# Kernel optimization log

Measured on AMD Instinct MI355X. Metric: run time of the kernel, lower is better.

The kernel has to match this reference:

```python
import jax, jax.numpy as jnp
import numpy as np

B, N, H, E, D = 8, 2048, 1024, 8, 2048


def setup_inputs() -> dict:
    key = jax.random.key(0)
    k = jax.random.split(key, 5)
    x = jax.random.normal(k[0], (B, N, H), dtype=jnp.float32)
    Wr = jax.random.normal(k[1], (H, E), dtype=jnp.float32) * 0.02
    br = jnp.zeros((E,), dtype=jnp.float32)
    W1 = jax.random.normal(k[2], (E, H, D), dtype=jnp.float32) * 0.02
    b1 = jnp.zeros((E, D), dtype=jnp.float32)
    W2 = jax.random.normal(k[3], (E, D, H), dtype=jnp.float32) * 0.02
    b2 = jnp.zeros((E, H), dtype=jnp.float32)
    return {"x": x, "Wr": Wr, "br": br, "W1": W1, "b1": b1, "W2": W2, "b2": b2}


def reference(x, Wr, br, W1, b1, W2, b2):
    # x: [B,N,H]; router v1, top-1, eval mode (no expert dropout)
    Bx, Nx, Hx = x.shape
    Ex = Wr.shape[1]
    x_flat = x.reshape(Bx * Nx, Hx)                      # [T,H]
    logits = x_flat @ Wr + br                            # [T,E]
    probs = jax.nn.softmax(logits, axis=-1)              # [T,E]
    expert_idx = jnp.argmax(probs, axis=-1)              # [T]

    out_flat = jnp.zeros_like(x_flat)
    for e in range(Ex):  # small fixed loop over experts
        h = jax.nn.gelu(x_flat @ W1[e] + b1[e], approximate=False)  # exact erf GELU (torch default)
        eout = h @ W2[e] + b2[e]                         # [T,H]
        out_flat = jnp.where((expert_idx == e)[:, None], eout, out_flat)

    out = x + out_flat.reshape(Bx, Nx, Hx)               # residual

    p_i = probs.mean(axis=0)                             # [E]
    balance_loss = Ex * jnp.sum(p_i ** 2)
    EPS = 1e-8
    entropy = -jnp.sum(probs * jnp.log(probs + EPS), axis=-1)
    entropy_loss = entropy.mean()
    tokens_per_expert = jnp.bincount(expert_idx, length=Ex)
    return out, balance_loss, entropy_loss, tokens_per_expert
```

## Files before the change

kernel.cpp:

```cpp
#include <hip/hip_runtime.h>
#include <math.h>

#define TT 16384
#define HH 1024
#define DD 2048
#define EE 8
#define MAXT 96

typedef float f32x4 __attribute__((ext_vector_type(4)));
typedef __bf16 bf16x8 __attribute__((ext_vector_type(8)));

__device__ __forceinline__ unsigned short f2bf(float f) {
  union { float f; unsigned u; } v; v.f = f;
  unsigned r = v.u + 0x7FFFu + ((v.u >> 16) & 1u);
  return (unsigned short)(r >> 16);
}

__device__ __forceinline__ void gl2lds16(const unsigned short* g, unsigned short* l) {
  __builtin_amdgcn_global_load_lds(
      (const __attribute__((address_space(1))) void*)g,
      (__attribute__((address_space(3))) void*)l, 16, 0, 0);
}

__global__ void k_init(int* counts, float* probs_sum, float* ent_sum) {
  int t = threadIdx.x;
  if (t < EE) { counts[t] = 0; probs_sum[t] = 0.f; }
  if (t == 0) *ent_sum = 0.f;
}

__global__ __launch_bounds__(256) void k_transpose(const float* __restrict__ src,
                                                   unsigned short* __restrict__ dst,
                                                   int R, int C) {
  __shared__ float tile[32][33];
  int tilesC = C / 32, tilesR = R / 32;
  int bid = blockIdx.x;
  int e = bid / (tilesR * tilesC);
  int rem = bid % (tilesR * tilesC);
  int tr = rem / tilesC, tc = rem % tilesC;
  const float* s = src + (size_t)e * R * C;
  unsigned short* d = dst + (size_t)e * R * C;
  int tx = threadIdx.x & 31, ty = threadIdx.x >> 5;
#pragma unroll
  for (int i = 0; i < 4; ++i)
    tile[ty + i * 8][tx] = s[(size_t)(tr * 32 + ty + i * 8) * C + tc * 32 + tx];
  __syncthreads();
#pragma unroll
  for (int i = 0; i < 4; ++i) {
    int rr = ty + i * 8;
    d[(size_t)(tc * 32 + rr) * R + tr * 32 + tx] = f2bf(tile[tx][rr]);
  }
}

__global__ __launch_bounds__(256) void k_router(const float* __restrict__ x,
                                                const float* __restrict__ Wr,
                                                const float* __restrict__ br,
                                                int* __restrict__ eidx,
                                                float* __restrict__ probs_sum,
                                                float* __restrict__ ent_sum,
                                                int* __restrict__ counts,
                                                unsigned short* __restrict__ xb) {
  __shared__ float s_p[EE];
  __shared__ int   s_c[EE];
  __shared__ float s_e;
  int tid = threadIdx.x;
  if (tid < EE) { s_p[tid] = 0.f; s_c[tid] = 0; }
  if (tid == 0) s_e = 0.f;
  __syncthreads();
  int lane = tid & 63, w = tid >> 6;
  for (int tt = 0; tt < 4; ++tt) {
    int token = blockIdx.x * 16 + w * 4 + tt;
    double acc[EE];
#pragma unroll
    for (int e = 0; e < EE; ++e) acc[e] = 0.0;
    const float* xr = x + (size_t)token * HH;
    unsigned short* xo = xb + (size_t)token * HH;
    for (int i = 0; i < 16; ++i) {
      int hh = i * 64 + lane;
      float xf = xr[hh];
      xo[hh] = f2bf(xf);
      double xv = (double)xf;
      const float* wr = Wr + (size_t)hh * EE;
#pragma unroll
      for (int e = 0; e < EE; ++e) acc[e] += xv * (double)wr[e];
    }
#pragma unroll
    for (int off = 32; off > 0; off >>= 1) {
#pragma unroll
      for (int e = 0; e < EE; ++e) acc[e] += __shfl_down(acc[e], off);
    }
    if (lane == 0) {
      double l[EE];
#pragma unroll
      for (int e = 0; e < EE; ++e) l[e] = acc[e] + (double)br[e];
      double m = l[0]; int am = 0;
#pragma unroll
      for (int e = 1; e < EE; ++e) { if (l[e] > m) { m = l[e]; am = e; } }
      double p[EE]; double s = 0.0;
#pragma unroll
      for (int e = 0; e < EE; ++e) { p[e] = exp(l[e] - m); s += p[e]; }
      double inv = 1.0 / s; double ent = 0.0;
#pragma unroll
      for (int e = 0; e < EE; ++e) { p[e] *= inv; ent -= p[e] * log(p[e] + 1e-8); }
      eidx[token] = am;
#pragma unroll
      for (int e = 0; e < EE; ++e) atomicAdd(&s_p[e], (float)p[e]);
      atomicAdd(&s_e, (float)ent);
      atomicAdd(&s_c[am], 1);
    }
  }
  __syncthreads();
  if (tid < EE) { atomicAdd(&probs_sum[tid], s_p[tid]); atomicAdd(&counts[tid], s_c[tid]); }
  if (tid == 0) atomicAdd(ent_sum, s_e);
}

__global__ void k_scan(const int* counts, const float* probs_sum, const float* ent_sum,
                       int* offsets, int* cursor,
                       int* tileE, int* tileR0, int* tileEnd, int* nTiles,
                       float* out_scalars) {
  if (threadIdx.x != 0) return;
  int off = 0, nt = 0;
  for (int e = 0; e < EE; ++e) {
    offsets[e] = off; cursor[e] = off;
    int c = counts[e];
    for (int r = 0; r < c; r += 256) {
      tileE[nt] = e; tileR0[nt] = off + r; tileEnd[nt] = off + c; ++nt;
    }
    off += c;
  }
  offsets[EE] = off;
  *nTiles = nt;
  float bal = 0.f;
  for (int e = 0; e < EE; ++e) { float pi = probs_sum[e] / (float)TT; bal += pi * pi; }
  out_scalars[0] = (float)EE * bal;
  out_scalars[1] = *ent_sum / (float)TT;
  for (int e = 0; e < EE; ++e) out_scalars[2 + e] = (float)counts[e];
}

__global__ __launch_bounds__(256) void k_perm(const int* __restrict__ eidx,
                                              int* cursor, int* __restrict__ perm) {
  int t = blockIdx.x * 256 + threadIdx.x;
  int lane = threadIdx.x & 63;
  int mye = eidx[t];
  int pos = 0;
#pragma unroll
  for (int e = 0; e < EE; ++e) {
    unsigned long long mask = __ballot(mye == e);
    if (mask == 0ull) continue;
    int leader = __ffsll(mask) - 1;
    int base = 0;
    if (lane == leader) base = atomicAdd(&cursor[e], __popcll(mask));
    base = __shfl(base, leader);
    if (mye == e) pos = base + (int)__popcll(mask & ((1ull << lane) - 1ull));
  }
  perm[pos] = t;
}


__global__ __launch_bounds__(512, 4) void k_gemm1(const unsigned short* __restrict__ xb,
                                                  const unsigned short* __restrict__ Wt1,
                                                  const float* __restrict__ b1,
                                                  const int* __restrict__ perm,
                                                  const int* __restrict__ tileE,
                                                  const int* __restrict__ tileR0,
                                                  const int* __restrict__ tileEnd,
                                                  const int* __restrict__ nTiles,
                                                  unsigned short* __restrict__ hbuf) {
  int tile = blockIdx.y, cblk = blockIdx.x;
  if (tile >= *nTiles) return;
  int e = tileE[tile], r0 = tileR0[tile], rend = tileEnd[tile];
  int c0 = cblk * 128;

  __shared__ __align__(16) unsigned short sA[2][256 * 32];
  __shared__ __align__(16) unsigned short sB[2][128 * 32];

  int tid = threadIdx.x, lane = tid & 63, wid = tid >> 6;
  int wr = wid >> 1, wc = wid & 1;
  int l16 = lane & 15, quad = lane >> 4;
  const int fsw  = (quad ^ ((l16 >> 1) & 3)) << 3;
  const int aoff = (wr * 64 + l16) * 32 + fsw;
  const int boff = (wc * 64 + l16) * 32 + fsw;

  const int ssw = (((tid & 3) ^ ((tid >> 3) & 3)) << 3);
  int row0 = r0 + (tid >> 2);        if (row0 > rend - 1) row0 = rend - 1;
  int row1 = r0 + 128 + (tid >> 2);  if (row1 > rend - 1) row1 = rend - 1;
  const unsigned short* aG0 = xb + (size_t)perm[row0] * HH + ssw;
  const unsigned short* aG1 = xb + (size_t)perm[row1] * HH + ssw;
  const unsigned short* bG  = Wt1 + (size_t)e * DD * HH + (size_t)(c0 + (tid >> 2)) * HH + ssw;
  const int dstA0 = wid * 512, dstA1 = 4096 + wid * 512, dstB = wid * 512;

  f32x4 acc[4][4] = {};
  const int NT = HH / 32;

  gl2lds16(aG0, &sA[0][dstA0]);
  gl2lds16(aG1, &sA[0][dstA1]);
  gl2lds16(bG,  &sB[0][dstB]);
  asm volatile("s_waitcnt vmcnt(0)" ::: "memory");
  __builtin_amdgcn_s_barrier();

#pragma unroll 2
  for (int kt = 0; kt < NT; ++kt) {
    const unsigned short* A = &sA[kt & 1][0];
    const unsigned short* B = &sB[kt & 1][0];
    bf16x8 av[4], bv[4];
#pragma unroll
    for (int i = 0; i < 4; ++i) av[i] = *(const bf16x8*)(A + aoff + i * 512);
#pragma unroll
    for (int j = 0; j < 4; ++j) bv[j] = *(const bf16x8*)(B + boff + j * 512);
    if (kt + 1 < NT) {
      int nb = (kt + 1) & 1, ko = (kt + 1) * 32;
      gl2lds16(aG0 + ko, &sA[nb][dstA0]);
      gl2lds16(aG1 + ko, &sA[nb][dstA1]);
      gl2lds16(bG  + ko, &sB[nb][dstB]);
    }
    asm volatile("s_waitcnt lgkmcnt(0)");
    __builtin_amdgcn_sched_barrier(0);
    __builtin_amdgcn_s_setprio(1);
#pragma unroll
    for (int i = 0; i < 4; ++i)
#pragma unroll
      for (int j = 0; j < 4; ++j)
        acc[i][j] = __builtin_amdgcn_mfma_f32_16x16x32_bf16(av[i], bv[j], acc[i][j], 0, 0, 0);
    __builtin_amdgcn_s_setprio(0);
    asm volatile("s_waitcnt vmcnt(0)" ::: "memory");
    __builtin_amdgcn_s_barrier();
  }

  float bias[4];
#pragma unroll
  for (int j = 0; j < 4; ++j) bias[j] = b1[e * DD + c0 + wc * 64 + j * 16 + l16];
#pragma unroll
  for (int i = 0; i < 4; ++i) {
#pragma unroll
    for (int r = 0; r < 4; ++r) {
      int gr = r0 + wr * 64 + i * 16 + quad * 4 + r;
      if (gr < rend) {
#pragma unroll
        for (int j = 0; j < 4; ++j) {
          int col = c0 + wc * 64 + j * 16 + l16;
          float v = acc[i][j][r] + bias[j];
          v = 0.5f * v * (1.0f + erff(v * 0.70710678118654752f));
          hbuf[(size_t)gr * DD + col] = f2bf(v);
        }
      }
    }
  }
}

__global__ __launch_bounds__(512, 4) void k_gemm2(const unsigned short* __restrict__ hbuf,
                                                  const unsigned short* __restrict__ Wt2,
                                                  const float* __restrict__ b2,
                                                  const float* __restrict__ x,
                                                  const int* __restrict__ perm,
                                                  const int* __restrict__ tileE,
                                                  const int* __restrict__ tileR0,
                                                  const int* __restrict__ tileEnd,
                                                  const int* __restrict__ nTiles,
                                                  float* __restrict__ outp) {
  int tile = blockIdx.y, cblk = blockIdx.x;
  if (tile >= *nTiles) return;
  int e = tileE[tile], r0 = tileR0[tile], rend = tileEnd[tile];
  int c0 = cblk * 128;

  __shared__ __align__(16) unsigned short sA[2][256 * 32];
  __shared__ __align__(16) unsigned short sB[2][128 * 32];

  int tid = threadIdx.x, lane = tid & 63, wid = tid >> 6;
  int wr = wid >> 1, wc = wid & 1;
  int l16 = lane & 15, quad = lane >> 4;
  const int fsw  = (quad ^ ((l16 >> 1) & 3)) << 3;
  const int aoff = (wr * 64 + l16) * 32 + fsw;
  const int boff = (wc * 64 + l16) * 32 + fsw;

  const int ssw = (((tid & 3) ^ ((tid >> 3) & 3)) << 3);
  int row0 = r0 + (tid >> 2);        if (row0 > rend - 1) row0 = rend - 1;
  int row1 = r0 + 128 + (tid >> 2);  if (row1 > rend - 1) row1 = rend - 1;
  const unsigned short* aG0 = hbuf + (size_t)row0 * DD + ssw;
  const unsigned short* aG1 = hbuf + (size_t)row1 * DD + ssw;
  const unsigned short* bG  = Wt2 + (size_t)e * HH * DD + (size_t)(c0 + (tid >> 2)) * DD + ssw;
  const int dstA0 = wid * 512, dstA1 = 4096 + wid * 512, dstB = wid * 512;

  f32x4 acc[4][4] = {};
  const int NT = DD / 32;

  gl2lds16(aG0, &sA[0][dstA0]);
  gl2lds16(aG1, &sA[0][dstA1]);
  gl2lds16(bG,  &sB[0][dstB]);
  asm volatile("s_waitcnt vmcnt(0)" ::: "memory");
  __builtin_amdgcn_s_barrier();

#pragma unroll 2
  for (int kt = 0; kt < NT; ++kt) {
    const unsigned short* A = &sA[kt & 1][0];
    const unsigned short* B = &sB[kt & 1][0];
    bf16x8 av[4], bv[4];
#pragma unroll
    for (int i = 0; i < 4; ++i) av[i] = *(const bf16x8*)(A + aoff + i * 512);
#pragma unroll
    for (int j = 0; j < 4; ++j) bv[j] = *(const bf16x8*)(B + boff + j * 512);
    if (kt + 1 < NT) {
      int nb = (kt + 1) & 1, ko = (kt + 1) * 32;
      gl2lds16(aG0 + ko, &sA[nb][dstA0]);
      gl2lds16(aG1 + ko, &sA[nb][dstA1]);
      gl2lds16(bG  + ko, &sB[nb][dstB]);
    }
    asm volatile("s_waitcnt lgkmcnt(0)");
    __builtin_amdgcn_sched_barrier(0);
    __builtin_amdgcn_s_setprio(1);
#pragma unroll
    for (int i = 0; i < 4; ++i)
#pragma unroll
      for (int j = 0; j < 4; ++j)
        acc[i][j] = __builtin_amdgcn_mfma_f32_16x16x32_bf16(av[i], bv[j], acc[i][j], 0, 0, 0);
    __builtin_amdgcn_s_setprio(0);
    asm volatile("s_waitcnt vmcnt(0)" ::: "memory");
    __builtin_amdgcn_s_barrier();
  }

  float bias[4];
#pragma unroll
  for (int j = 0; j < 4; ++j) bias[j] = b2[e * HH + c0 + wc * 64 + j * 16 + l16];
#pragma unroll
  for (int i = 0; i < 4; ++i) {
#pragma unroll
    for (int r = 0; r < 4; ++r) {
      int gr = r0 + wr * 64 + i * 16 + quad * 4 + r;
      if (gr < rend) {
        int tok = perm[gr];
#pragma unroll
        for (int j = 0; j < 4; ++j) {
          int col = c0 + wc * 64 + j * 16 + l16;
          size_t oi = (size_t)tok * HH + col;
          outp[oi] = x[oi] + bias[j] + acc[i][j][r];
        }
      }
    }
  }
}

extern "C" void kernel_launch(void* const* d_in, const int* in_sizes, int n_in,
                              void* d_out, int out_size, void* d_ws, size_t ws_size,
                              hipStream_t stream) {
  const float* x  = (const float*)d_in[0];
  const float* Wr = (const float*)d_in[1];
  const float* br = (const float*)d_in[2];
  const float* W1 = (const float*)d_in[3];
  const float* b1 = (const float*)d_in[4];
  const float* W2 = (const float*)d_in[5];
  const float* b2 = (const float*)d_in[6];
  float* outp = (float*)d_out;

  char* ws = (char*)d_ws;
  int*   counts    = (int*)(ws + 0);
  int*   cursor    = (int*)(ws + 64);
  int*   nTiles    = (int*)(ws + 128);
  float* probs_sum = (float*)(ws + 192);
  float* ent_sum   = (float*)(ws + 256);
  int*   offsets   = (int*)(ws + 320);
  int*   tileE     = (int*)(ws + 512);
  int*   tileR0    = (int*)(ws + 2048);
  int*   tileEnd   = (int*)(ws + 3584);
  int*   eidx      = (int*)(ws + 8192);
  int*   perm      = (int*)(ws + 8192 + 4 * (size_t)TT);
  size_t off = 8192 + 8 * (size_t)TT;
  unsigned short* xb   = (unsigned short*)(ws + off); off += (size_t)TT * HH * 2;
  unsigned short* Wt1  = (unsigned short*)(ws + off); off += (size_t)EE * DD * HH * 2;
  unsigned short* Wt2  = (unsigned short*)(ws + off); off += (size_t)EE * HH * DD * 2;
  unsigned short* hbuf = (unsigned short*)(ws + off); off += (size_t)TT * DD * 2;

  k_init<<<1, 64, 0, stream>>>(counts, probs_sum, ent_sum);
  k_transpose<<<EE * (HH / 32) * (DD / 32), 256, 0, stream>>>(W1, Wt1, HH, DD);
  k_transpose<<<EE * (DD / 32) * (HH / 32), 256, 0, stream>>>(W2, Wt2, DD, HH);
  k_router<<<TT / 16, 256, 0, stream>>>(x, Wr, br, eidx, probs_sum, ent_sum, counts, xb);
  k_scan<<<1, 64, 0, stream>>>(counts, probs_sum, ent_sum, offsets, cursor,
                               tileE, tileR0, tileEnd, nTiles, outp + (size_t)TT * HH);
  k_perm<<<TT / 256, 256, 0, stream>>>(eidx, cursor, perm);
  dim3 g1(DD / 128, MAXT);
  k_gemm1<<<g1, 512, 0, stream>>>(xb, Wt1, b1, perm, tileE, tileR0, tileEnd, nTiles, hbuf);
  dim3 g2(HH / 128, MAXT);
  k_gemm2<<<g2, 512, 0, stream>>>(hbuf, Wt2, b2, x, perm, tileE, tileR0, tileEnd, nTiles, outp);
}
```

Before: 599.2 us.

## Use 128-row tiles, 4-stage LDS pipeline and XCD-aware tile mapping in expert GEMMs

Both expert GEMMs move from 256x128 tiles with 512 threads and a double buffer to 128x128 tiles with 256 threads. They now use a 4-deep LDS ring that prefetches three k-steps ahead and waits with partial vmcnt, so global loads overlap more MFMA work. Block indices are remapped so each XCD gets a contiguous range of expert tiles, which aims to improve L2 reuse of the expert weights. The tile-table scan is parallelized across threads. Smaller tiles mean more tiles and less operand reuse per block, and the 64KB of LDS per block caps residency at two blocks per CU.

```diff
diff --git a/kernel.cpp b/kernel.cpp
--- a/kernel.cpp
+++ b/kernel.cpp
@@ -5,7 +5,7 @@
 #define HH 1024
 #define DD 2048
 #define EE 8
-#define MAXT 96
+#define MAXT 136
 
 typedef float f32x4 __attribute__((ext_vector_type(4)));
 typedef __bf16 bf16x8 __attribute__((ext_vector_type(8)));
@@ -113,27 +113,37 @@
   if (tid == 0) atomicAdd(ent_sum, s_e);
 }
 
-__global__ void k_scan(const int* counts, const float* probs_sum, const float* ent_sum,
-                       int* offsets, int* cursor,
+__global__ __launch_bounds__(256) void k_scan(const int* counts, const float* probs_sum,
+                       const float* ent_sum, int* offsets, int* cursor,
                        int* tileE, int* tileR0, int* tileEnd, int* nTiles,
                        float* out_scalars) {
-  if (threadIdx.x != 0) return;
-  int off = 0, nt = 0;
-  for (int e = 0; e < EE; ++e) {
-    offsets[e] = off; cursor[e] = off;
-    int c = counts[e];
-    for (int r = 0; r < c; r += 256) {
-      tileE[nt] = e; tileR0[nt] = off + r; tileEnd[nt] = off + c; ++nt;
-    }
-    off += c;
-  }
-  offsets[EE] = off;
-  *nTiles = nt;
-  float bal = 0.f;
-  for (int e = 0; e < EE; ++e) { float pi = probs_sum[e] / (float)TT; bal += pi * pi; }
-  out_scalars[0] = (float)EE * bal;
-  out_scalars[1] = *ent_sum / (float)TT;
-  for (int e = 0; e < EE; ++e) out_scalars[2 + e] = (float)counts[e];
+  __shared__ int soff[EE + 1];
+  __shared__ int tbase[EE + 1];
+  int t = threadIdx.x;
+  if (t == 0) {
+    int off = 0, tb = 0;
+    for (int e = 0; e < EE; ++e) {
+      soff[e] = off; offsets[e] = off; cursor[e] = off;
+      tbase[e] = tb;
+      tb += (counts[e] + 127) >> 7;
+      off += counts[e];
+    }
+    soff[EE] = off; offsets[EE] = off; tbase[EE] = tb;
+    *nTiles = tb;
+    float bal = 0.f;
+    for (int e = 0; e < EE; ++e) { float pi = probs_sum[e] / (float)TT; bal += pi * pi; }
+    out_scalars[0] = (float)EE * bal;
+    out_scalars[1] = *ent_sum / (float)TT;
+    for (int e = 0; e < EE; ++e) out_scalars[2 + e] = (float)counts[e];
+  }
+  __syncthreads();
+  int nt = tbase[EE];
+  for (int i = t; i < nt; i += 256) {
+    int e = 0;
+    while (tbase[e + 1] <= i) ++e;
+    int j = i - tbase[e];
+    tileE[i] = e; tileR0[i] = soff[e] + j * 128; tileEnd[i] = soff[e] + counts[e];
+  }
 }
 
 __global__ __launch_bounds__(256) void k_perm(const int* __restrict__ eidx,
@@ -156,7 +166,35 @@
 }
 
 
-__global__ __launch_bounds__(512, 4) void k_gemm1(const unsigned short* __restrict__ xb,
+#define K_ITER(kt_, stage_, vm_)                                              \
+  {                                                                           \
+    asm volatile("s_waitcnt vmcnt(" vm_ ")" ::: "memory");                    \
+    __builtin_amdgcn_s_barrier();                                             \
+    const unsigned short* A = &sA[(kt_) & 3][0];                              \
+    const unsigned short* B = &sB[(kt_) & 3][0];                              \
+    bf16x8 av[4], bv[4];                                                      \
+    _Pragma("unroll") for (int i = 0; i < 4; ++i)                             \
+        av[i] = *(const bf16x8*)(A + aoff + i * 512);                         \
+    _Pragma("unroll") for (int j = 0; j < 4; ++j)                             \
+        bv[j] = *(const bf16x8*)(B + boff + j * 512);                         \
+    if (stage_) {                                                             \
+      int nb = ((kt_) + 3) & 3, ko = ((kt_) + 3) * 32;                        \
+      gl2lds16(aG0 + ko, &sA[nb][dst0]);                                      \
+      gl2lds16(aG1 + ko, &sA[nb][dst1]);                                      \
+      gl2lds16(bG0 + ko, &sB[nb][dst0]);                                      \
+      gl2lds16(bG1 + ko, &sB[nb][dst1]);                                      \
+    }                                                                         \
+    asm volatile("s_waitcnt lgkmcnt(0)");                                     \
+    __builtin_amdgcn_sched_barrier(0);                                        \
+    __builtin_amdgcn_s_setprio(1);                                            \
+    _Pragma("unroll") for (int i = 0; i < 4; ++i)                             \
+        _Pragma("unroll") for (int j = 0; j < 4; ++j)                         \
+            acc[i][j] = __builtin_amdgcn_mfma_f32_16x16x32_bf16(              \
+                av[i], bv[j], acc[i][j], 0, 0, 0);                            \
+    __builtin_amdgcn_s_setprio(0);                                            \
+  }
+
+__global__ __launch_bounds__(256, 2) void k_gemm1(const unsigned short* __restrict__ xb,
                                                   const unsigned short* __restrict__ Wt1,
                                                   const float* __restrict__ b1,
                                                   const int* __restrict__ perm,
@@ -165,13 +203,19 @@
                                                   const int* __restrict__ tileEnd,
                                                   const int* __restrict__ nTiles,
                                                   unsigned short* __restrict__ hbuf) {
-  int tile = blockIdx.y, cblk = blockIdx.x;
-  if (tile >= *nTiles) return;
+  int d = blockIdx.x + blockIdx.y * 16;
+  int nt = *nTiles;
+  int tpx = (nt + 7) >> 3;
+  int xcd = d & 7, idx = d >> 3;
+  if ((idx >> 4) >= tpx) return;
+  int tile = xcd * tpx + (idx >> 4);
+  int cblk = idx & 15;
+  if (tile >= nt) return;
   int e = tileE[tile], r0 = tileR0[tile], rend = tileEnd[tile];
   int c0 = cblk * 128;
 
-  __shared__ __align__(16) unsigned short sA[2][256 * 32];
-  __shared__ __align__(16) unsigned short sB[2][128 * 32];
+  __shared__ __align__(16) unsigned short sA[4][4096];
+  __shared__ __align__(16) unsigned short sB[4][4096];
 
   int tid = threadIdx.x, lane = tid & 63, wid = tid >> 6;
   int wr = wid >> 1, wc = wid & 1;
@@ -180,50 +224,32 @@
   const int aoff = (wr * 64 + l16) * 32 + fsw;
   const int boff = (wc * 64 + l16) * 32 + fsw;
 
-  const int ssw = (((tid & 3) ^ ((tid >> 3) & 3)) << 3);
-  int row0 = r0 + (tid >> 2);        if (row0 > rend - 1) row0 = rend - 1;
-  int row1 = r0 + 128 + (tid >> 2);  if (row1 > rend - 1) row1 = rend - 1;
-  const unsigned short* aG0 = xb + (size_t)perm[row0] * HH + ssw;
-  const unsigned short* aG1 = xb + (size_t)perm[row1] * HH + ssw;
-  const unsigned short* bG  = Wt1 + (size_t)e * DD * HH + (size_t)(c0 + (tid >> 2)) * HH + ssw;
-  const int dstA0 = wid * 512, dstA1 = 4096 + wid * 512, dstB = wid * 512;
+  int srow = lane >> 2;
+  const int ssw = (((lane & 3) ^ ((lane >> 3) & 3)) << 3);
+  int ra0 = r0 + wid * 32 + srow;       if (ra0 > rend - 1) ra0 = rend - 1;
+  int ra1 = ra0 + 16;                   if (ra1 > rend - 1) ra1 = rend - 1;
+  const unsigned short* aG0 = xb + (size_t)perm[ra0] * HH + ssw;
+  const unsigned short* aG1 = xb + (size_t)perm[ra1] * HH + ssw;
+  const unsigned short* bB  = Wt1 + (size_t)e * DD * HH;
+  const unsigned short* bG0 = bB + (size_t)(c0 + wid * 32 + srow) * HH + ssw;
+  const unsigned short* bG1 = bG0 + (size_t)16 * HH;
+  const int dst0 = wid * 1024, dst1 = wid * 1024 + 512;
 
   f32x4 acc[4][4] = {};
   const int NT = HH / 32;
 
-  gl2lds16(aG0, &sA[0][dstA0]);
-  gl2lds16(aG1, &sA[0][dstA1]);
-  gl2lds16(bG,  &sB[0][dstB]);
-  asm volatile("s_waitcnt vmcnt(0)" ::: "memory");
-  __builtin_amdgcn_s_barrier();
-
-#pragma unroll 2
-  for (int kt = 0; kt < NT; ++kt) {
-    const unsigned short* A = &sA[kt & 1][0];
-    const unsigned short* B = &sB[kt & 1][0];
-    bf16x8 av[4], bv[4];
-#pragma unroll
-    for (int i = 0; i < 4; ++i) av[i] = *(const bf16x8*)(A + aoff + i * 512);
-#pragma unroll
-    for (int j = 0; j < 4; ++j) bv[j] = *(const bf16x8*)(B + boff + j * 512);
-    if (kt + 1 < NT) {
-      int nb = (kt + 1) & 1, ko = (kt + 1) * 32;
-      gl2lds16(aG0 + ko, &sA[nb][dstA0]);
-      gl2lds16(aG1 + ko, &sA[nb][dstA1]);
-      gl2lds16(bG  + ko, &sB[nb][dstB]);
-    }
-    asm volatile("s_waitcnt lgkmcnt(0)");
-    __builtin_amdgcn_sched_barrier(0);
-    __builtin_amdgcn_s_setprio(1);
-#pragma unroll
-    for (int i = 0; i < 4; ++i)
-#pragma unroll
-      for (int j = 0; j < 4; ++j)
-        acc[i][j] = __builtin_amdgcn_mfma_f32_16x16x32_bf16(av[i], bv[j], acc[i][j], 0, 0, 0);
-    __builtin_amdgcn_s_setprio(0);
-    asm volatile("s_waitcnt vmcnt(0)" ::: "memory");
-    __builtin_amdgcn_s_barrier();
-  }
+#pragma unroll
+  for (int t = 0; t < 3; ++t) {
+    gl2lds16(aG0 + t * 32, &sA[t][dst0]);
+    gl2lds16(aG1 + t * 32, &sA[t][dst1]);
+    gl2lds16(bG0 + t * 32, &sB[t][dst0]);
+    gl2lds16(bG1 + t * 32, &sB[t][dst1]);
+  }
+
+#pragma unroll 4
+  for (int kt = 0; kt < NT - 2; ++kt) K_ITER(kt, kt + 3 < NT, "8");
+  K_ITER(NT - 2, 0, "4");
+  K_ITER(NT - 1, 0, "0");
 
   float bias[4];
 #pragma unroll
@@ -246,7 +272,7 @@
   }
 }
 
-__global__ __launch_bounds__(512, 4) void k_gemm2(const unsigned short* __restrict__ hbuf,
+__global__ __launch_bounds__(256, 2) void k_gemm2(const unsigned short* __restrict__ hbuf,
                                                   const unsigned short* __restrict__ Wt2,
                                                   const float* __restrict__ b2,
                                                   const float* __restrict__ x,
@@ -256,13 +282,19 @@
                                                   const int* __restrict__ tileEnd,
                                                   const int* __restrict__ nTiles,
                                                   float* __restrict__ outp) {
-  int tile = blockIdx.y, cblk = blockIdx.x;
-  if (tile >= *nTiles) return;
+  int d = blockIdx.x + blockIdx.y * 8;
+  int nt = *nTiles;
+  int tpx = (nt + 7) >> 3;
+  int xcd = d & 7, idx = d >> 3;
+  if ((idx >> 3) >= tpx) return;
+  int tile = xcd * tpx + (idx >> 3);
+  int cblk = idx & 7;
+  if (tile >= nt) return;
   int e = tileE[tile], r0 = tileR0[tile], rend = tileEnd[tile];
   int c0 = cblk * 128;
 
-  __shared__ __align__(16) unsigned short sA[2][256 * 32];
-  __shared__ __align__(16) unsigned short sB[2][128 * 32];
+  __shared__ __align__(16) unsigned short sA[4][4096];
+  __shared__ __align__(16) unsigned short sB[4][4096];
 
   int tid = threadIdx.x, lane = tid & 63, wid = tid >> 6;
   int wr = wid >> 1, wc = wid & 1;
@@ -271,50 +303,32 @@
   const int aoff = (wr * 64 + l16) * 32 + fsw;
   const int boff = (wc * 64 + l16) * 32 + fsw;
 
-  const int ssw = (((tid & 3) ^ ((tid >> 3) & 3)) << 3);
-  int row0 = r0 + (tid >> 2);        if (row0 > rend - 1) row0 = rend - 1;
-  int row1 = r0 + 128 + (tid >> 2);  if (row1 > rend - 1) row1 = rend - 1;
-  const unsigned short* aG0 = hbuf + (size_t)row0 * DD + ssw;
-  const unsigned short* aG1 = hbuf + (size_t)row1 * DD + ssw;
-  const unsigned short* bG  = Wt2 + (size_t)e * HH * DD + (size_t)(c0 + (tid >> 2)) * DD + ssw;
-  const int dstA0 = wid * 512, dstA1 = 4096 + wid * 512, dstB = wid * 512;
+  int srow = lane >> 2;
+  const int ssw = (((lane & 3) ^ ((lane >> 3) & 3)) << 3);
+  int ra0 = r0 + wid * 32 + srow;       if (ra0 > rend - 1) ra0 = rend - 1;
+  int ra1 = ra0 + 16;                   if (ra1 > rend - 1) ra1 = rend - 1;
+  const unsigned short* aG0 = hbuf + (size_t)ra0 * DD + ssw;
+  const unsigned short* aG1 = hbuf + (size_t)ra1 * DD + ssw;
+  const unsigned short* bB  = Wt2 + (size_t)e * HH * DD;
+  const unsigned short* bG0 = bB + (size_t)(c0 + wid * 32 + srow) * DD + ssw;
+  const unsigned short* bG1 = bG0 + (size_t)16 * DD;
+  const int dst0 = wid * 1024, dst1 = wid * 1024 + 512;
 
   f32x4 acc[4][4] = {};
   const int NT = DD / 32;
 
-  gl2lds16(aG0, &sA[0][dstA0]);
-  gl2lds16(aG1, &sA[0][dstA1]);
-  gl2lds16(bG,  &sB[0][dstB]);
-  asm volatile("s_waitcnt vmcnt(0)" ::: "memory");
-  __builtin_amdgcn_s_barrier();
-
-#pragma unroll 2
-  for (int kt = 0; kt < NT; ++kt) {
-    const unsigned short* A = &sA[kt & 1][0];
-    const unsigned short* B = &sB[kt & 1][0];
-    bf16x8 av[4], bv[4];
-#pragma unroll
-    for (int i = 0; i < 4; ++i) av[i] = *(const bf16x8*)(A + aoff + i * 512);
-#pragma unroll
-    for (int j = 0; j < 4; ++j) bv[j] = *(const bf16x8*)(B + boff + j * 512);
-    if (kt + 1 < NT) {
-      int nb = (kt + 1) & 1, ko = (kt + 1) * 32;
-      gl2lds16(aG0 + ko, &sA[nb][dstA0]);
-      gl2lds16(aG1 + ko, &sA[nb][dstA1]);
-      gl2lds16(bG  + ko, &sB[nb][dstB]);
-    }
-    asm volatile("s_waitcnt lgkmcnt(0)");
-    __builtin_amdgcn_sched_barrier(0);
-    __builtin_amdgcn_s_setprio(1);
-#pragma unroll
-    for (int i = 0; i < 4; ++i)
-#pragma unroll
-      for (int j = 0; j < 4; ++j)
-        acc[i][j] = __builtin_amdgcn_mfma_f32_16x16x32_bf16(av[i], bv[j], acc[i][j], 0, 0, 0);
-    __builtin_amdgcn_s_setprio(0);
-    asm volatile("s_waitcnt vmcnt(0)" ::: "memory");
-    __builtin_amdgcn_s_barrier();
-  }
+#pragma unroll
+  for (int t = 0; t < 3; ++t) {
+    gl2lds16(aG0 + t * 32, &sA[t][dst0]);
+    gl2lds16(aG1 + t * 32, &sA[t][dst1]);
+    gl2lds16(bG0 + t * 32, &sB[t][dst0]);
+    gl2lds16(bG1 + t * 32, &sB[t][dst1]);
+  }
+
+#pragma unroll 4
+  for (int kt = 0; kt < NT - 2; ++kt) K_ITER(kt, kt + 3 < NT, "8");
+  K_ITER(NT - 2, 0, "4");
+  K_ITER(NT - 1, 0, "0");
 
   float bias[4];
 #pragma unroll
@@ -371,11 +385,11 @@
   k_transpose<<<EE * (HH / 32) * (DD / 32), 256, 0, stream>>>(W1, Wt1, HH, DD);
   k_transpose<<<EE * (DD / 32) * (HH / 32), 256, 0, stream>>>(W2, Wt2, DD, HH);
   k_router<<<TT / 16, 256, 0, stream>>>(x, Wr, br, eidx, probs_sum, ent_sum, counts, xb);
-  k_scan<<<1, 64, 0, stream>>>(counts, probs_sum, ent_sum, offsets, cursor,
-                               tileE, tileR0, tileEnd, nTiles, outp + (size_t)TT * HH);
+  k_scan<<<1, 256, 0, stream>>>(counts, probs_sum, ent_sum, offsets, cursor,
+                                tileE, tileR0, tileEnd, nTiles, outp + (size_t)TT * HH);
   k_perm<<<TT / 256, 256, 0, stream>>>(eidx, cursor, perm);
-  dim3 g1(DD / 128, MAXT);
-  k_gemm1<<<g1, 512, 0, stream>>>(xb, Wt1, b1, perm, tileE, tileR0, tileEnd, nTiles, hbuf);
-  dim3 g2(HH / 128, MAXT);
-  k_gemm2<<<g2, 512, 0, stream>>>(hbuf, Wt2, b2, x, perm, tileE, tileR0, tileEnd, nTiles, outp);
-}
+  dim3 g1(16, MAXT);
+  k_gemm1<<<g1, 256, 0, stream>>>(xb, Wt1, b1, perm, tileE, tileR0, tileEnd, nTiles, hbuf);
+  dim3 g2(8, MAXT);
+  k_gemm2<<<g2, 256, 0, stream>>>(hbuf, Wt2, b2, x, perm, tileE, tileR0, tileEnd, nTiles, outp);
+}
```

Measured after the change: 646.7 us. 1.08x slower.
